# Kernel tuning notes

Measured on AMD Instinct MI355X. Metric: run time of the kernel, lower is better.

## Reference

```python
import jax, jax.numpy as jnp
import numpy as np

MARGIN = 6.0
EPSILON = 2.0
REL_DIM = 256
REL_RANGE = (MARGIN + EPSILON) / REL_DIM  # OpenKE rel_embedding_range = 0.03125
PI = 3.14159265358979323846


def setup_inputs() -> dict:
    key = jax.random.key(0)
    k1, k2, k3, k4, k5 = jax.random.split(key, 5)
    B, S, H = 16, 64, 768
    E, D2 = 43234, 512  # entity count, entity embed dim (2*256)
    return {
        "question_hidden": jax.random.normal(k1, (B, S, H), dtype=jnp.float32),
        "W_rel": jax.random.normal(k2, (18, H), dtype=jnp.float32) * 0.02,
        "b_rel": jnp.zeros((18,), dtype=jnp.float32),
        "rel_embeddings": jax.random.normal(k3, (18, REL_DIM), dtype=jnp.float32) * REL_RANGE,
        "ent_embeddings": jax.random.normal(k4, (E, D2), dtype=jnp.float32) * 0.05,
        "head_id": jax.random.randint(k5, (B,), 0, E, dtype=jnp.int64),
    }


def reference(question_hidden, W_rel, b_rel, rel_embeddings, ent_embeddings, head_id):
    # RelationPredictor: mean-pool BERT hidden states, then Linear(768 -> 18)
    q = jnp.mean(question_hidden, axis=1)                       # (B, 768)
    rel_scores = q @ W_rel.T + b_rel                            # (B, 18)
    # soft relation mixture -> predicted relation embedding
    predict_relation = jax.nn.sigmoid(rel_scores) @ rel_embeddings  # (B, 256)
    head = ent_embeddings[head_id]                              # (B, 512)
    re_h, im_h = jnp.split(head, 2, axis=-1)                    # (B, 256) each
    phase = predict_relation / (REL_RANGE / PI)
    re_r, im_r = jnp.cos(phase), jnp.sin(phase)
    # rotate head by relation (complex multiply)
    rot_re = re_h * re_r - im_h * im_r                          # (B, 256)
    rot_im = re_h * im_r + im_h * re_r                          # (B, 256)
    re_t, im_t = jnp.split(ent_embeddings, 2, axis=-1)          # (E, 256) each
    # broadcast distance vs all entities: (B, E, 256) intermediates
    dre = rot_re[:, None, :] - re_t[None, :, :]
    dim_ = rot_im[:, None, :] - im_t[None, :, :]
    dist = jnp.sqrt(dre * dre + dim_ * dim_).sum(axis=-1)       # (B, E)
    return MARGIN - dist
```

## Files before the change

kernel.cpp:

```cpp
#include <hip/hip_runtime.h>
#include <hip/hip_bf16.h>
#include <math.h>

#define MARGIN_F 6.0f
#define PHASE_SCALE 100.53096491487338f

__global__ void k_prep(const float* __restrict__ qh, const float* __restrict__ W,
                       const float* __restrict__ brel,
                       const float* __restrict__ rel,
                       const float* __restrict__ ent, const int* __restrict__ hid,
                       float* __restrict__ rot) {
    __shared__ float q[768];
    __shared__ float sig[18];
    int b = blockIdx.x;
    int t = threadIdx.x;

    if (t < 768) {
        float s = 0.f;
        const float* base = qh + (size_t)b * 64 * 768 + t;
        #pragma unroll 8
        for (int srow = 0; srow < 64; ++srow) s += base[(size_t)srow * 768];
        q[t] = s * (1.0f / 64.0f);
    }
    __syncthreads();

    int wave = t >> 6, lane = t & 63;
    for (int r = wave; r < 18; r += 16) {
        float p = 0.f;
        for (int h = lane; h < 768; h += 64) p += q[h] * W[r * 768 + h];
        for (int off = 32; off; off >>= 1) p += __shfl_xor(p, off, 64);
        if (lane == 0) sig[r] = 1.0f / (1.0f + expf(-(p + brel[r])));
    }
    __syncthreads();

    if (t < 256) {
        int d = t;
        float pr = 0.f;
        #pragma unroll
        for (int r = 0; r < 18; ++r) pr += sig[r] * rel[r * 256 + d];
        float phase = pr * PHASE_SCALE;
        float sn, cs;
        sincosf(phase, &sn, &cs);
        int h0 = hid[b];
        float reh = ent[(size_t)h0 * 512 + d];
        float imh = ent[(size_t)h0 * 512 + 256 + d];
        rot[b * 256 + d]        = reh * cs - imh * sn;
        rot[4096 + b * 256 + d] = reh * sn + imh * cs;
    }
}

__global__ __launch_bounds__(256, 4) void k_dist(const float* __restrict__ ent,
                                                 const float* __restrict__ rot,
                                                 float* __restrict__ out, int E,
                                                 int chunk) {
    int lane = threadIdx.x & 63;
    int w4 = threadIdx.x >> 6;

    const float4* rre4 = (const float4*)rot + (size_t)w4 * 4 * 64;
    const float4* rim4 = (const float4*)(rot + 4096) + (size_t)w4 * 4 * 64;
    float4 ra[4], ia[4];
    #pragma unroll
    for (int b = 0; b < 4; ++b) {
        ra[b] = rre4[b * 64 + lane];
        ia[b] = rim4[b * 64 + lane];
    }

    int bout = w4 * 4 + (((lane & 1) << 1) | ((lane >> 1) & 1));

    int e0 = blockIdx.x * chunk;
    int e1 = min(e0 + chunk, E);

    for (int e = e0; e < e1; ++e) {
        const float4* r4 = (const float4*)(ent + (size_t)e * 512);
        float4 te = r4[lane];
        float4 ti = r4[64 + lane];

        float v[4];
        #pragma unroll
        for (int b = 0; b < 4; ++b) {
            float dx0 = ra[b].x - te.x, dy0 = ia[b].x - ti.x;
            float dx1 = ra[b].y - te.y, dy1 = ia[b].y - ti.y;
            float dx2 = ra[b].z - te.z, dy2 = ia[b].z - ti.z;
            float dx3 = ra[b].w - te.w, dy3 = ia[b].w - ti.w;
            float s0 = __builtin_amdgcn_sqrtf(dx0 * dx0 + dy0 * dy0);
            float s1 = __builtin_amdgcn_sqrtf(dx1 * dx1 + dy1 * dy1);
            float s2 = __builtin_amdgcn_sqrtf(dx2 * dx2 + dy2 * dy2);
            float s3 = __builtin_amdgcn_sqrtf(dx3 * dx3 + dy3 * dy3);
            v[b] = (s0 + s1) + (s2 + s3);
        }

        #pragma unroll
        for (int i = 0; i < 2; ++i) {
            float send = (lane & 1) ? v[i] : v[i + 2];
            float recv = __shfl_xor(send, 1, 64);
            v[i] = ((lane & 1) ? v[i + 2] : v[i]) + recv;
        }
        {
            float send = (lane & 2) ? v[0] : v[1];
            float recv = __shfl_xor(send, 2, 64);
            v[0] = ((lane & 2) ? v[1] : v[0]) + recv;
        }
        v[0] += __shfl_xor(v[0], 4, 64);
        v[0] += __shfl_xor(v[0], 8, 64);
        v[0] += __shfl_xor(v[0], 16, 64);
        v[0] += __shfl_xor(v[0], 32, 64);

        if (lane < 4) out[(size_t)bout * E + e] = MARGIN_F - v[0];
    }
}

extern "C" void kernel_launch(void* const* d_in, const int* in_sizes, int n_in,
                              void* d_out, int out_size, void* d_ws,
                              size_t ws_size, hipStream_t stream) {
    const float* qh   = (const float*)d_in[0];
    const float* W    = (const float*)d_in[1];
    const float* brel = (const float*)d_in[2];
    const float* rel  = (const float*)d_in[3];
    const float* ent  = (const float*)d_in[4];
    const int*   hid  = (const int*)d_in[5];
    float* out = (float*)d_out;

    int E = in_sizes[4] / 512;

    float* rot = (float*)d_ws;

    k_prep<<<dim3(16), 1024, 0, stream>>>(qh, W, brel, rel, ent, hid, rot);

    const int NB = 2048;
    int chunk = (E + NB - 1) / NB;
    k_dist<<<dim3(NB), 256, 0, stream>>>(ent, rot, out, E, chunk);
}
```

Baseline: 57.25 us.

## Process four entities per group with software-pipelined transpose-reduce and stores

Each wave now loads four entity rows per group, so it computes 16 partial sums and reduces them with a butterfly transpose that needs fewer shuffles per entity. Two register sets alternate so that computing one group overlaps the shuffle reduction and store of the previous one. Empty blocks now exit early, and inline asm barriers pin the rotated-head vectors in VGPRs. The cost is higher register pressure under launch bounds of 256 threads with 4 waves, plus redundant clamped loads at the chunk tail.

```diff
diff --git a/kernel.cpp b/kernel.cpp
--- a/kernel.cpp
+++ b/kernel.cpp
@@ -64,49 +64,89 @@
         ra[b] = rre4[b * 64 + lane];
         ia[b] = rim4[b * 64 + lane];
     }
+    #pragma unroll
+    for (int b = 0; b < 4; ++b) {
+        asm volatile("" : "+v"(ra[b].x), "+v"(ra[b].y), "+v"(ra[b].z), "+v"(ra[b].w));
+        asm volatile("" : "+v"(ia[b].x), "+v"(ia[b].y), "+v"(ia[b].z), "+v"(ia[b].w));
+    }
 
-    int bout = w4 * 4 + (((lane & 1) << 1) | ((lane >> 1) & 1));
+    int eoff = (((lane & 1) << 1) | ((lane >> 1) & 1));
+    int bout = w4 * 4 + ((((lane >> 2) & 1) << 1) | ((lane >> 3) & 1));
 
     int e0 = blockIdx.x * chunk;
+    if (e0 >= E) return;
     int e1 = min(e0 + chunk, E);
 
-    for (int e = e0; e < e1; ++e) {
-        const float4* r4 = (const float4*)(ent + (size_t)e * 512);
-        float4 te = r4[lane];
-        float4 ti = r4[64 + lane];
+#define COMPUTE(V, EB)                                                        \
+    {                                                                         \
+        _Pragma("unroll") for (int g_ = 0; g_ < 4; ++g_) {                    \
+            int ee_ = min((EB) + g_, e1 - 1);                                 \
+            const float4* r4_ = (const float4*)(ent + (size_t)ee_ * 512);     \
+            float4 te_ = r4_[lane];                                           \
+            float4 ti_ = r4_[64 + lane];                                      \
+            _Pragma("unroll") for (int b_ = 0; b_ < 4; ++b_) {                \
+                float dx0 = ra[b_].x - te_.x, dy0 = ia[b_].x - ti_.x;         \
+                float dx1 = ra[b_].y - te_.y, dy1 = ia[b_].y - ti_.y;         \
+                float dx2 = ra[b_].z - te_.z, dy2 = ia[b_].z - ti_.z;         \
+                float dx3 = ra[b_].w - te_.w, dy3 = ia[b_].w - ti_.w;         \
+                float s0 = __builtin_amdgcn_sqrtf(dx0 * dx0 + dy0 * dy0);     \
+                float s1 = __builtin_amdgcn_sqrtf(dx1 * dx1 + dy1 * dy1);     \
+                float s2 = __builtin_amdgcn_sqrtf(dx2 * dx2 + dy2 * dy2);     \
+                float s3 = __builtin_amdgcn_sqrtf(dx3 * dx3 + dy3 * dy3);     \
+                V[g_ * 4 + b_] = (s0 + s1) + (s2 + s3);                       \
+            }                                                                 \
+        }                                                                     \
+    }
 
-        float v[4];
-        #pragma unroll
-        for (int b = 0; b < 4; ++b) {
-            float dx0 = ra[b].x - te.x, dy0 = ia[b].x - ti.x;
-            float dx1 = ra[b].y - te.y, dy1 = ia[b].y - ti.y;
-            float dx2 = ra[b].z - te.z, dy2 = ia[b].z - ti.z;
-            float dx3 = ra[b].w - te.w, dy3 = ia[b].w - ti.w;
-            float s0 = __builtin_amdgcn_sqrtf(dx0 * dx0 + dy0 * dy0);
-            float s1 = __builtin_amdgcn_sqrtf(dx1 * dx1 + dy1 * dy1);
-            float s2 = __builtin_amdgcn_sqrtf(dx2 * dx2 + dy2 * dy2);
-            float s3 = __builtin_amdgcn_sqrtf(dx3 * dx3 + dy3 * dy3);
-            v[b] = (s0 + s1) + (s2 + s3);
-        }
+#define RSTORE(V, EB)                                                         \
+    {                                                                         \
+        _Pragma("unroll") for (int i_ = 0; i_ < 8; ++i_) {                    \
+            float s_ = (lane & 1) ? V[i_] : V[i_ + 8];                        \
+            float c_ = __shfl_xor(s_, 1, 64);                                 \
+            V[i_] = ((lane & 1) ? V[i_ + 8] : V[i_]) + c_;                    \
+        }                                                                     \
+        _Pragma("unroll") for (int i_ = 0; i_ < 4; ++i_) {                    \
+            float s_ = (lane & 2) ? V[i_] : V[i_ + 4];                        \
+            float c_ = __shfl_xor(s_, 2, 64);                                 \
+            V[i_] = ((lane & 2) ? V[i_ + 4] : V[i_]) + c_;                    \
+        }                                                                     \
+        _Pragma("unroll") for (int i_ = 0; i_ < 2; ++i_) {                    \
+            float s_ = (lane & 4) ? V[i_] : V[i_ + 2];                        \
+            float c_ = __shfl_xor(s_, 4, 64);                                 \
+            V[i_] = ((lane & 4) ? V[i_ + 2] : V[i_]) + c_;                    \
+        }                                                                     \
+        {                                                                     \
+            float s_ = (lane & 8) ? V[0] : V[1];                              \
+            float c_ = __shfl_xor(s_, 8, 64);                                 \
+            V[0] = ((lane & 8) ? V[1] : V[0]) + c_;                           \
+        }                                                                     \
+        V[0] += __shfl_xor(V[0], 16, 64);                                     \
+        V[0] += __shfl_xor(V[0], 32, 64);                                     \
+        if (lane < 16 && (EB) + eoff < e1)                                    \
+            out[(size_t)bout * E + (EB) + eoff] = MARGIN_F - V[0];            \
+    }
 
-        #pragma unroll
-        for (int i = 0; i < 2; ++i) {
-            float send = (lane & 1) ? v[i] : v[i + 2];
-            float recv = __shfl_xor(send, 1, 64);
-            v[i] = ((lane & 1) ? v[i + 2] : v[i]) + recv;
-        }
-        {
-            float send = (lane & 2) ? v[0] : v[1];
-            float recv = __shfl_xor(send, 2, 64);
-            v[0] = ((lane & 2) ? v[1] : v[0]) + recv;
-        }
-        v[0] += __shfl_xor(v[0], 4, 64);
-        v[0] += __shfl_xor(v[0], 8, 64);
-        v[0] += __shfl_xor(v[0], 16, 64);
-        v[0] += __shfl_xor(v[0], 32, 64);
+    int ngroups = (e1 - e0 + 3) >> 2;
+    float vA[16], vB[16];
 
-        if (lane < 4) out[(size_t)bout * E + e] = MARGIN_F - v[0];
+    COMPUTE(vA, e0);
+    int g = 1;
+    for (; g + 1 < ngroups; g += 2) {
+        COMPUTE(vB, e0 + g * 4);
+        RSTORE(vA, e0 + (g - 1) * 4);
+        COMPUTE(vA, e0 + (g + 1) * 4);
+        RSTORE(vB, e0 + g * 4);
     }
+    if (g < ngroups) {
+        COMPUTE(vB, e0 + g * 4);
+        RSTORE(vA, e0 + (g - 1) * 4);
+        RSTORE(vB, e0 + g * 4);
+    } else {
+        RSTORE(vA, e0 + (ngroups - 1) * 4);
+    }
+
+#undef COMPUTE
+#undef RSTORE
 }
 
 extern "C" void kernel_launch(void* const* d_in, const int* in_sizes, int n_in,
```

New measurement: 59.23 us. 3.5% more time.
